# Kernel optimization log

Hardware: AMD Instinct MI355X
Metric: run time of the kernel (lower is better)

Reference implementation:

```python
import jax, jax.numpy as jnp
import numpy as np

T, H, I, E, K = 4096, 2048, 4096, 8, 2

def setup_inputs() -> dict:
    key = jax.random.key(0)
    k1, k2, k3, k4, k5 = jax.random.split(key, 5)
    return {
        "hidden_states": jax.random.normal(k1, (T, H), dtype=jnp.float32),
        "topk_weights": jax.random.uniform(k2, (T, K), dtype=jnp.float32, minval=0.01, maxval=1.0),
        "topk_ids": jax.random.randint(k3, (T, K), 0, E, dtype=jnp.int64),
        "gate_up_weights": jax.random.normal(k4, (E, 2 * I, H), dtype=jnp.float32) * 0.02,
        "down_weights": jax.random.normal(k5, (E, H, I), dtype=jnp.float32) * 0.02,
    }

def reference(hidden_states, topk_weights, topk_ids, gate_up_weights, down_weights):
    # renormalize=True: per-token top-k weights sum to 1
    tw = topk_weights / jnp.sum(topk_weights, axis=-1, keepdims=True)  # [T, K]
    n_experts = gate_up_weights.shape[0]
    # per-expert combine weight for each token: sum of tw where routed to expert e -> [E, T]
    expert_w = jax.vmap(
        lambda e: jnp.sum(jnp.where(topk_ids == e, tw, 0.0), axis=-1)
    )(jnp.arange(n_experts))

    def body(acc, ew):
        gu, dw, w = ew  # gu: [2I, H], dw: [H, I], w: [T]
        h = hidden_states @ gu.T            # [T, 2I]
        gate, up = jnp.split(h, 2, axis=-1)  # silu_and_mul epilogue
        act = jax.nn.silu(gate) * up        # [T, I]
        out_e = act @ dw.T                  # [T, H]
        return acc + w[:, None] * out_e, None

    init = jnp.zeros_like(hidden_states)
    out, _ = jax.lax.scan(body, init, (gate_up_weights, down_weights, expert_w))
    return out
```

## Files before the change

kernel.cpp:

```cpp
#include <hip/hip_runtime.h>


#define T_TOK 4096
#define H_DIM 2048
#define I_DIM 4096
#define E_NUM 8
#define K_TOP 2
#define NSLOT (T_TOK * K_TOP)

#define BM 128
#define BN 128
#define BK 64
#define LDK 72

typedef float f32x4 __attribute__((ext_vector_type(4)));
typedef __bf16 bf16x8 __attribute__((ext_vector_type(8)));
typedef unsigned int u32x4 __attribute__((ext_vector_type(4)));

static __device__ __forceinline__ unsigned short f2bf(float f) {
  unsigned u = __float_as_uint(f);
  u += 0x7FFFu + ((u >> 16) & 1u);
  return (unsigned short)(u >> 16);
}

static __device__ __forceinline__ unsigned long long pack4bf(float x0, float x1, float x2, float x3) {
  unsigned lo = (unsigned)f2bf(x0) | ((unsigned)f2bf(x1) << 16);
  unsigned hi = (unsigned)f2bf(x2) | ((unsigned)f2bf(x3) << 16);
  return (unsigned long long)lo | ((unsigned long long)hi << 32);
}

static __device__ __forceinline__ void gload16(void* lds, const void* g) {
  __builtin_amdgcn_global_load_lds(
      (const __attribute__((address_space(1))) unsigned int*)(g),
      (__attribute__((address_space(3))) unsigned int*)(lds), 16, 0, 0);
}

__global__ void routing_kernel(const float* __restrict__ tw,
                               const int* __restrict__ ids,
                               int* __restrict__ offsets,
                               int* __restrict__ stok,
                               float* __restrict__ sw,
                               int* __restrict__ slot_of) {
  __shared__ int cnt[E_NUM];
  __shared__ int cur[E_NUM];
  __shared__ int basesh[E_NUM + 1];
  int tid = threadIdx.x;
  if (tid < E_NUM) cnt[tid] = 0;
  __syncthreads();
  for (int idx = tid; idx < NSLOT; idx += 256) atomicAdd(&cnt[ids[idx]], 1);
  __syncthreads();
  if (tid == 0) {
    int acc = 0;
    for (int e = 0; e < E_NUM; ++e) { basesh[e] = acc; acc += cnt[e]; }
    basesh[E_NUM] = acc;
    for (int e = 0; e <= E_NUM; ++e) offsets[e] = basesh[e];
  }
  __syncthreads();
  if (tid < E_NUM) cur[tid] = basesh[tid];
  __syncthreads();
  for (int idx = tid; idx < NSLOT; idx += 256) {
    int t = idx >> 1;
    float w0 = tw[t * 2], w1 = tw[t * 2 + 1];
    float w = ((idx & 1) ? w1 : w0) / (w0 + w1);
    int e = ids[idx];
    int slot = atomicAdd(&cur[e], 1);
    stok[slot] = t;
    sw[slot] = w;
    slot_of[idx] = slot;
  }
}

__global__ __launch_bounds__(256) void cvt_bf16_kernel(const float* __restrict__ in,
                                                       unsigned short* __restrict__ out,
                                                       long long n8) {
  long long stride = (long long)gridDim.x * 256;
  for (long long i = (long long)blockIdx.x * 256 + threadIdx.x; i < n8; i += stride) {
    long long o = i * 8;
    f32x4 v0 = *(const f32x4*)(in + o);
    f32x4 v1 = *(const f32x4*)(in + o + 4);
    unsigned long long p0 = pack4bf(v0[0], v0[1], v0[2], v0[3]);
    unsigned long long p1 = pack4bf(v1[0], v1[1], v1[2], v1[3]);
    u32x4 st;
    st[0] = (unsigned)p0; st[1] = (unsigned)(p0 >> 32);
    st[2] = (unsigned)p1; st[3] = (unsigned)(p1 >> 32);
    *(u32x4*)(out + o) = st;
  }
}

__global__ __launch_bounds__(256, 2) void gemm1_bf16_kernel(
    const unsigned short* __restrict__ hb,
    const unsigned short* __restrict__ gub,
    const int* __restrict__ offsets, const int* __restrict__ stok,
    unsigned short* __restrict__ act) {
  int e = blockIdx.z;
  int base = offsets[e];
  int cnt = offsets[e + 1] - base;
  int m0 = blockIdx.y * BM;
  if (m0 >= cnt) return;
  int n0 = blockIdx.x * BN;
  int rem = cnt - m0;

  __shared__ __attribute__((aligned(16))) unsigned short As[BM * 64];
  __shared__ __attribute__((aligned(16))) unsigned short Bg[BN * 64];
  __shared__ __attribute__((aligned(16))) unsigned short Bu[BN * 64];
  __shared__ int toks[BM];

  int tid = threadIdx.x;
  if (tid < BM) toks[tid] = (tid < rem) ? stok[base + m0 + tid] : stok[base];
  __syncthreads();

  int lane = tid & 63;
  int wid = tid >> 6;
  int srow = lane >> 3;
  int scol = ((lane & 7) ^ srow) << 3;

  const unsigned short* wrow = gub + (size_t)e * (2 * (size_t)I_DIM) * H_DIM;
  const unsigned short* pa[4];
  const unsigned short* pg[4];
  const unsigned short* pu[4];
#pragma unroll
  for (int s = 0; s < 4; ++s) {
    int row = wid * 32 + s * 8 + srow;
    pa[s] = hb + (size_t)toks[row] * H_DIM + scol;
    pg[s] = wrow + (size_t)(n0 + row) * H_DIM + scol;
    pu[s] = wrow + (size_t)(I_DIM + n0 + row) * H_DIM + scol;
  }

  int lm = lane & 15;
  int q = lane >> 4;
  int wm = (wid >> 1) * 64;
  int wn = (wid & 1) * 64;
  int rc0 = ((q ^ (lm & 7)) << 3);
  int rc1 = (((4 + q) ^ (lm & 7)) << 3);

  f32x4 accg[4][4] = {};
  f32x4 accu[4][4] = {};

  for (int kb = 0; kb < H_DIM; kb += BK) {
#pragma unroll
    for (int s = 0; s < 4; ++s) {
      gload16(&As[(wid * 32 + s * 8) * 64], pa[s] + kb);
      gload16(&Bg[(wid * 32 + s * 8) * 64], pg[s] + kb);
      gload16(&Bu[(wid * 32 + s * 8) * 64], pu[s] + kb);
    }
    __syncthreads();
#pragma unroll
    for (int ks = 0; ks < 2; ++ks) {
      int ko = ks ? rc1 : rc0;
      bf16x8 a[4], bg[4], bu[4];
#pragma unroll
      for (int i = 0; i < 4; ++i)
        a[i] = *(const bf16x8*)&As[(wm + i * 16 + lm) * 64 + ko];
#pragma unroll
      for (int j = 0; j < 4; ++j) {
        bg[j] = *(const bf16x8*)&Bg[(wn + j * 16 + lm) * 64 + ko];
        bu[j] = *(const bf16x8*)&Bu[(wn + j * 16 + lm) * 64 + ko];
      }
#pragma unroll
      for (int i = 0; i < 4; ++i)
#pragma unroll
        for (int j = 0; j < 4; ++j) {
          accg[i][j] = __builtin_amdgcn_mfma_f32_16x16x32_bf16(a[i], bg[j], accg[i][j], 0, 0, 0);
          accu[i][j] = __builtin_amdgcn_mfma_f32_16x16x32_bf16(a[i], bu[j], accu[i][j], 0, 0, 0);
        }
    }
    __syncthreads();
  }

#pragma unroll
  for (int i = 0; i < 4; ++i) {
    int mb = wm + i * 16 + q * 4;
#pragma unroll
    for (int r = 0; r < 4; ++r) {
      int m = mb + r;
      if (m < rem) {
        size_t rowoff = (size_t)(base + m0 + m) * I_DIM + n0;
#pragma unroll
        for (int j = 0; j < 4; ++j) {
          int n = wn + j * 16 + lm;
          float g = accg[i][j][r];
          float u = accu[i][j][r];
          float aa = (g / (1.0f + __expf(-g))) * u;
          act[rowoff + n] = f2bf(aa);
        }
      }
    }
  }
}

__global__ __launch_bounds__(256, 2) void gemm2_bf16_kernel(
    const unsigned short* __restrict__ act, const unsigned short* __restrict__ dwb,
    const int* __restrict__ offsets, const float* __restrict__ sw,
    float* __restrict__ dout) {
  int e = blockIdx.z;
  int base = offsets[e];
  int cnt = offsets[e + 1] - base;
  int m0 = blockIdx.y * BM;
  if (m0 >= cnt) return;
  int n0 = blockIdx.x * BN;
  int rem = cnt - m0;

  __shared__ __attribute__((aligned(16))) unsigned short As[BM * 64];
  __shared__ __attribute__((aligned(16))) unsigned short Bs[BN * 64];
  __shared__ float wsl[BM];

  int tid = threadIdx.x;
  if (tid < BM) wsl[tid] = (tid < rem) ? sw[base + m0 + tid] : 0.f;

  int lane = tid & 63;
  int wid = tid >> 6;
  int srow = lane >> 3;
  int scol = ((lane & 7) ^ srow) << 3;

  const unsigned short* dp = dwb + (size_t)e * ((size_t)H_DIM * I_DIM);
  const unsigned short* pa[4];
  const unsigned short* pb[4];
#pragma unroll
  for (int s = 0; s < 4; ++s) {
    int row = wid * 32 + s * 8 + srow;
    pa[s] = act + (size_t)(base + m0 + row) * I_DIM + scol;
    pb[s] = dp + (size_t)(n0 + row) * I_DIM + scol;
  }

  int lm = lane & 15;
  int q = lane >> 4;
  int wm = (wid >> 1) * 64;
  int wn = (wid & 1) * 64;
  int rc0 = ((q ^ (lm & 7)) << 3);
  int rc1 = (((4 + q) ^ (lm & 7)) << 3);

  f32x4 acc[4][4] = {};

  for (int kb = 0; kb < I_DIM; kb += BK) {
#pragma unroll
    for (int s = 0; s < 4; ++s) {
      gload16(&As[(wid * 32 + s * 8) * 64], pa[s] + kb);
      gload16(&Bs[(wid * 32 + s * 8) * 64], pb[s] + kb);
    }
    __syncthreads();
#pragma unroll
    for (int ks = 0; ks < 2; ++ks) {
      int ko = ks ? rc1 : rc0;
      bf16x8 a[4], b[4];
#pragma unroll
      for (int i = 0; i < 4; ++i)
        a[i] = *(const bf16x8*)&As[(wm + i * 16 + lm) * 64 + ko];
#pragma unroll
      for (int j = 0; j < 4; ++j)
        b[j] = *(const bf16x8*)&Bs[(wn + j * 16 + lm) * 64 + ko];
#pragma unroll
      for (int i = 0; i < 4; ++i)
#pragma unroll
        for (int j = 0; j < 4; ++j)
          acc[i][j] = __builtin_amdgcn_mfma_f32_16x16x32_bf16(a[i], b[j], acc[i][j], 0, 0, 0);
    }
    __syncthreads();
  }

#pragma unroll
  for (int i = 0; i < 4; ++i) {
    int mb = wm + i * 16 + q * 4;
#pragma unroll
    for (int r = 0; r < 4; ++r) {
      int m = mb + r;
      if (m < rem) {
        float w = wsl[m];
        size_t rowoff = (size_t)(base + m0 + m) * H_DIM + n0;
#pragma unroll
        for (int j = 0; j < 4; ++j)
          dout[rowoff + wn + j * 16 + lm] = acc[i][j][r] * w;
      }
    }
  }
}

__global__ __launch_bounds__(256, 2) void gemm1_kernel(
    const float* __restrict__ hidden, const float* __restrict__ gu,
    const int* __restrict__ offsets, const int* __restrict__ stok,
    unsigned short* __restrict__ act) {
  int e = blockIdx.z;
  int base = offsets[e];
  int cnt = offsets[e + 1] - base;
  int m0 = blockIdx.y * BM;
  if (m0 >= cnt) return;
  int n0 = blockIdx.x * BN;
  int rem = cnt - m0;

  __shared__ unsigned short As[BM * LDK];
  __shared__ unsigned short Bg[BM * LDK];
  __shared__ unsigned short Bu[BM * LDK];
  __shared__ int toks[BM];

  int tid = threadIdx.x;
  if (tid < BM) toks[tid] = (tid < rem) ? stok[base + m0 + tid] : -1;
  __syncthreads();

  int lane = tid & 63;
  int wid = tid >> 6;
  int wm = (wid >> 1) * 64;
  int wn = (wid & 1) * 64;
  int lm = lane & 15;
  int q = lane >> 4;

  f32x4 accg[4][4] = {};
  f32x4 accu[4][4] = {};
  const float* gup = gu + (size_t)e * (2 * (size_t)I_DIM * H_DIM);

  for (int kb = 0; kb < H_DIM; kb += BK) {
#pragma unroll
    for (int s = 0; s < 8; ++s) {
      int task = tid + s * 256;
      int row = task >> 4;
      int cg = (task & 15) << 2;
      int tok = toks[row];
      float x0 = 0.f, x1 = 0.f, x2 = 0.f, x3 = 0.f;
      if (tok >= 0) {
        f32x4 v = *(const f32x4*)(hidden + (size_t)tok * H_DIM + kb + cg);
        x0 = v[0]; x1 = v[1]; x2 = v[2]; x3 = v[3];
      }
      *(unsigned long long*)&As[row * LDK + cg] = pack4bf(x0, x1, x2, x3);
    }
#pragma unroll
    for (int s = 0; s < 8; ++s) {
      int task = tid + s * 256;
      int row = task >> 4;
      int cg = (task & 15) << 2;
      f32x4 vg = *(const f32x4*)(gup + (size_t)(n0 + row) * H_DIM + kb + cg);
      f32x4 vu = *(const f32x4*)(gup + (size_t)(I_DIM + n0 + row) * H_DIM + kb + cg);
      *(unsigned long long*)&Bg[row * LDK + cg] = pack4bf(vg[0], vg[1], vg[2], vg[3]);
      *(unsigned long long*)&Bu[row * LDK + cg] = pack4bf(vu[0], vu[1], vu[2], vu[3]);
    }
    __syncthreads();
#pragma unroll
    for (int ks = 0; ks < 2; ++ks) {
      int ko = ks * 32 + q * 8;
      bf16x8 a[4], bg[4], bu[4];
#pragma unroll
      for (int i = 0; i < 4; ++i)
        a[i] = *(const bf16x8*)&As[(wm + i * 16 + lm) * LDK + ko];
#pragma unroll
      for (int j = 0; j < 4; ++j) {
        bg[j] = *(const bf16x8*)&Bg[(wn + j * 16 + lm) * LDK + ko];
        bu[j] = *(const bf16x8*)&Bu[(wn + j * 16 + lm) * LDK + ko];
      }
#pragma unroll
      for (int i = 0; i < 4; ++i)
#pragma unroll
        for (int j = 0; j < 4; ++j) {
          accg[i][j] = __builtin_amdgcn_mfma_f32_16x16x32_bf16(a[i], bg[j], accg[i][j], 0, 0, 0);
          accu[i][j] = __builtin_amdgcn_mfma_f32_16x16x32_bf16(a[i], bu[j], accu[i][j], 0, 0, 0);
        }
    }
    __syncthreads();
  }

#pragma unroll
  for (int i = 0; i < 4; ++i) {
    int mb = wm + i * 16 + q * 4;
#pragma unroll
    for (int r = 0; r < 4; ++r) {
      int m = mb + r;
      if (m < rem) {
        size_t rowoff = (size_t)(base + m0 + m) * I_DIM + n0;
#pragma unroll
        for (int j = 0; j < 4; ++j) {
          int n = wn + j * 16 + lm;
          float g = accg[i][j][r];
          float u = accu[i][j][r];
          float aa = (g / (1.0f + __expf(-g))) * u;
          act[rowoff + n] = f2bf(aa);
        }
      }
    }
  }
}

__global__ __launch_bounds__(256, 2) void gemm2_kernel(
    const unsigned short* __restrict__ act, const float* __restrict__ dwn,
    const int* __restrict__ offsets, const float* __restrict__ sw,
    float* __restrict__ dout) {
  int e = blockIdx.z;
  int base = offsets[e];
  int cnt = offsets[e + 1] - base;
  int m0 = blockIdx.y * BM;
  if (m0 >= cnt) return;
  int n0 = blockIdx.x * BN;
  int rem = cnt - m0;

  __shared__ unsigned short As[BM * LDK];
  __shared__ unsigned short Bs[BM * LDK];
  __shared__ float wsl[BM];

  int tid = threadIdx.x;
  if (tid < BM) wsl[tid] = (tid < rem) ? sw[base + m0 + tid] : 0.f;

  int lane = tid & 63;
  int wid = tid >> 6;
  int wm = (wid >> 1) * 64;
  int wn = (wid & 1) * 64;
  int lm = lane & 15;
  int q = lane >> 4;

  f32x4 acc[4][4] = {};
  const float* dp = dwn + (size_t)e * ((size_t)H_DIM * I_DIM);
  const unsigned short* ap = act + (size_t)(base + m0) * I_DIM;

  for (int kb = 0; kb < I_DIM; kb += BK) {
#pragma unroll
    for (int s = 0; s < 4; ++s) {
      int task = tid + s * 256;
      int row = task >> 3;
      int cg = (task & 7) << 3;
      u32x4 v = *(const u32x4*)(ap + (size_t)row * I_DIM + kb + cg);
      *(u32x4*)&As[row * LDK + cg] = v;
    }
#pragma unroll
    for (int s = 0; s < 8; ++s) {
      int task = tid + s * 256;
      int row = task >> 4;
      int cg = (task & 15) << 2;
      f32x4 v = *(const f32x4*)(dp + (size_t)(n0 + row) * I_DIM + kb + cg);
      *(unsigned long long*)&Bs[row * LDK + cg] = pack4bf(v[0], v[1], v[2], v[3]);
    }
    __syncthreads();
#pragma unroll
    for (int ks = 0; ks < 2; ++ks) {
      int ko = ks * 32 + q * 8;
      bf16x8 a[4], b[4];
#pragma unroll
      for (int i = 0; i < 4; ++i)
        a[i] = *(const bf16x8*)&As[(wm + i * 16 + lm) * LDK + ko];
#pragma unroll
      for (int j = 0; j < 4; ++j)
        b[j] = *(const bf16x8*)&Bs[(wn + j * 16 + lm) * LDK + ko];
#pragma unroll
      for (int i = 0; i < 4; ++i)
#pragma unroll
        for (int j = 0; j < 4; ++j)
          acc[i][j] = __builtin_amdgcn_mfma_f32_16x16x32_bf16(a[i], b[j], acc[i][j], 0, 0, 0);
    }
    __syncthreads();
  }

#pragma unroll
  for (int i = 0; i < 4; ++i) {
    int mb = wm + i * 16 + q * 4;
#pragma unroll
    for (int r = 0; r < 4; ++r) {
      int m = mb + r;
      if (m < rem) {
        float w = wsl[m];
        size_t rowoff = (size_t)(base + m0 + m) * H_DIM + n0;
#pragma unroll
        for (int j = 0; j < 4; ++j)
          dout[rowoff + wn + j * 16 + lm] = acc[i][j][r] * w;
      }
    }
  }
}

__global__ void combine_kernel(const f32x4* __restrict__ dout4,
                               const int* __restrict__ slot_of,
                               f32x4* __restrict__ out4) {
  int idx = blockIdx.x * 256 + threadIdx.x;
  int t = idx >> 9;
  int c = idx & 511;
  int s0 = slot_of[t * 2];
  int s1 = slot_of[t * 2 + 1];
  f32x4 r = dout4[(size_t)s0 * 512 + c] + dout4[(size_t)s1 * 512 + c];
  out4[idx] = r;
}

extern "C" void kernel_launch(void* const* d_in, const int* in_sizes, int n_in,
                              void* d_out, int out_size, void* d_ws, size_t ws_size,
                              hipStream_t stream) {
  const float* hidden = (const float*)d_in[0];
  const float* tw     = (const float*)d_in[1];
  const int*   ids    = (const int*)d_in[2];
  const float* gu     = (const float*)d_in[3];
  const float* dwn    = (const float*)d_in[4];
  float* out = (float*)d_out;
  char* ws = (char*)d_ws;

  int*   offsets = (int*)ws;
  int*   stok    = (int*)(ws + 256);
  float* swp     = (float*)(ws + 256 + 32768);
  int*   slot_of = (int*)(ws + 256 + 65536);
  const size_t base_off = 1 << 17;
  const size_t act_sz   = (size_t)(NSLOT + BM) * I_DIM * 2;

  routing_kernel<<<1, 256, 0, stream>>>(tw, ids, offsets, stok, swp, slot_of);

  const size_t hb_sz  = (size_t)T_TOK * H_DIM * 2;
  const size_t gu_sz  = (size_t)E_NUM * 2 * (size_t)I_DIM * H_DIM * 2;
  const size_t dwn_sz = (size_t)E_NUM * (size_t)H_DIM * I_DIM * 2;
  const size_t w_off  = base_off + hb_sz;
  const size_t need   = w_off + gu_sz + act_sz;

  if (ws_size >= need) {
    unsigned short* hb   = (unsigned short*)(ws + base_off);
    unsigned short* gub  = (unsigned short*)(ws + w_off);
    unsigned short* dwb  = (unsigned short*)(ws + w_off);
    float*          dout = (float*)(ws + w_off + dwn_sz);
    unsigned short* act  = (unsigned short*)(ws + w_off + gu_sz);

    cvt_bf16_kernel<<<4096, 256, 0, stream>>>(hidden, hb, (long long)T_TOK * H_DIM / 8);
    cvt_bf16_kernel<<<8192, 256, 0, stream>>>(gu, gub, (long long)E_NUM * 2 * I_DIM * H_DIM / 8);
    gemm1_bf16_kernel<<<dim3(I_DIM / BN, NSLOT / BM, E_NUM), 256, 0, stream>>>(hb, gub, offsets, stok, act);
    cvt_bf16_kernel<<<8192, 256, 0, stream>>>(dwn, dwb, (long long)E_NUM * H_DIM * I_DIM / 8);
    gemm2_bf16_kernel<<<dim3(H_DIM / BN, NSLOT / BM, E_NUM), 256, 0, stream>>>(act, dwb, offsets, swp, dout);
    combine_kernel<<<(T_TOK * H_DIM / 4) / 256, 256, 0, stream>>>((const f32x4*)dout, slot_of, (f32x4*)out);
  } else {
    unsigned short* act  = (unsigned short*)(ws + base_off);
    float*          dout = (float*)(ws + base_off + act_sz);
    gemm1_kernel<<<dim3(I_DIM / BN, NSLOT / BM, E_NUM), 256, 0, stream>>>(hidden, gu, offsets, stok, act);
    gemm2_kernel<<<dim3(H_DIM / BN, NSLOT / BM, E_NUM), 256, 0, stream>>>(act, dwn, offsets, swp, dout);
    combine_kernel<<<(T_TOK * H_DIM / 4) / 256, 256, 0, stream>>>((const f32x4*)dout, slot_of, (f32x4*)out);
  }
}
```

Before: 1.480 ms.

## Double-buffer LDS tiles with BK=32 prefetch in bf16 expert GEMMs

Converts the bf16 gate-up and down GEMM kernels from a single-buffered BK=64 load/sync/compute loop to a double-buffered BK=32 loop. The next K-slice is issued to the alternate LDS buffer before computing on the current one, so there is one barrier per iteration instead of two. Each kernel keeps about the same LDS footprint. The swizzle is reworked for 32-wide rows, and gemm2's launch bounds rise to 3 blocks per CU to allow more occupancy. The trade-off is twice as many loop iterations and barriers per K range, and possible register pressure from the higher occupancy target. The fp32 fallback kernels only get the renamed stride constant and a hardcoded 64-step.

Measured after the change: 1.607 ms. 8.6% more time.

```diff
diff --git a/kernel.cpp b/kernel.cpp
--- a/kernel.cpp
+++ b/kernel.cpp
@@ -10,8 +10,8 @@
 
 #define BM 128
 #define BN 128
-#define BK 64
-#define LDK 72
+#define BK 32
+#define LDKO 72
 
 typedef float f32x4 __attribute__((ext_vector_type(4)));
 typedef __bf16 bf16x8 __attribute__((ext_vector_type(8)));
@@ -100,9 +100,9 @@
   int n0 = blockIdx.x * BN;
   int rem = cnt - m0;
 
-  __shared__ __attribute__((aligned(16))) unsigned short As[BM * 64];
-  __shared__ __attribute__((aligned(16))) unsigned short Bg[BN * 64];
-  __shared__ __attribute__((aligned(16))) unsigned short Bu[BN * 64];
+  __shared__ __attribute__((aligned(16))) unsigned short As[2][BM * BK];
+  __shared__ __attribute__((aligned(16))) unsigned short Bg[2][BN * BK];
+  __shared__ __attribute__((aligned(16))) unsigned short Bu[2][BN * BK];
   __shared__ int toks[BM];
 
   int tid = threadIdx.x;
@@ -111,60 +111,70 @@
 
   int lane = tid & 63;
   int wid = tid >> 6;
-  int srow = lane >> 3;
-  int scol = ((lane & 7) ^ srow) << 3;
+  int sr = lane >> 2;
+  int scz = ((lane & 3) ^ (sr & 3)) << 3;
 
   const unsigned short* wrow = gub + (size_t)e * (2 * (size_t)I_DIM) * H_DIM;
-  const unsigned short* pa[4];
-  const unsigned short* pg[4];
-  const unsigned short* pu[4];
-#pragma unroll
-  for (int s = 0; s < 4; ++s) {
-    int row = wid * 32 + s * 8 + srow;
-    pa[s] = hb + (size_t)toks[row] * H_DIM + scol;
-    pg[s] = wrow + (size_t)(n0 + row) * H_DIM + scol;
-    pu[s] = wrow + (size_t)(I_DIM + n0 + row) * H_DIM + scol;
+  const unsigned short* pa[2];
+  const unsigned short* pg[2];
+  const unsigned short* pu[2];
+  int lb[2];
+#pragma unroll
+  for (int s = 0; s < 2; ++s) {
+    int grp = (wid * 2 + s) * 16;
+    int row = grp + sr;
+    pa[s] = hb + (size_t)toks[row] * H_DIM + scz;
+    pg[s] = wrow + (size_t)(n0 + row) * H_DIM + scz;
+    pu[s] = wrow + (size_t)(I_DIM + n0 + row) * H_DIM + scz;
+    lb[s] = grp * BK;
   }
 
   int lm = lane & 15;
   int q = lane >> 4;
   int wm = (wid >> 1) * 64;
   int wn = (wid & 1) * 64;
-  int rc0 = ((q ^ (lm & 7)) << 3);
-  int rc1 = (((4 + q) ^ (lm & 7)) << 3);
+  int rcs = ((q ^ (lm & 3)) << 3);
 
   f32x4 accg[4][4] = {};
   f32x4 accu[4][4] = {};
 
+#pragma unroll
+  for (int s = 0; s < 2; ++s) {
+    gload16(&As[0][lb[s]], pa[s]);
+    gload16(&Bg[0][lb[s]], pg[s]);
+    gload16(&Bu[0][lb[s]], pu[s]);
+  }
+  __syncthreads();
+
+  int cur = 0;
   for (int kb = 0; kb < H_DIM; kb += BK) {
-#pragma unroll
-    for (int s = 0; s < 4; ++s) {
-      gload16(&As[(wid * 32 + s * 8) * 64], pa[s] + kb);
-      gload16(&Bg[(wid * 32 + s * 8) * 64], pg[s] + kb);
-      gload16(&Bu[(wid * 32 + s * 8) * 64], pu[s] + kb);
-    }
+    if (kb + BK < H_DIM) {
+      int nk = kb + BK;
+#pragma unroll
+      for (int s = 0; s < 2; ++s) {
+        gload16(&As[cur ^ 1][lb[s]], pa[s] + nk);
+        gload16(&Bg[cur ^ 1][lb[s]], pg[s] + nk);
+        gload16(&Bu[cur ^ 1][lb[s]], pu[s] + nk);
+      }
+    }
+    bf16x8 a[4], bg[4], bu[4];
+#pragma unroll
+    for (int i = 0; i < 4; ++i)
+      a[i] = *(const bf16x8*)&As[cur][(wm + i * 16 + lm) * BK + rcs];
+#pragma unroll
+    for (int j = 0; j < 4; ++j) {
+      bg[j] = *(const bf16x8*)&Bg[cur][(wn + j * 16 + lm) * BK + rcs];
+      bu[j] = *(const bf16x8*)&Bu[cur][(wn + j * 16 + lm) * BK + rcs];
+    }
+#pragma unroll
+    for (int i = 0; i < 4; ++i)
+#pragma unroll
+      for (int j = 0; j < 4; ++j) {
+        accg[i][j] = __builtin_amdgcn_mfma_f32_16x16x32_bf16(a[i], bg[j], accg[i][j], 0, 0, 0);
+        accu[i][j] = __builtin_amdgcn_mfma_f32_16x16x32_bf16(a[i], bu[j], accu[i][j], 0, 0, 0);
+      }
     __syncthreads();
-#pragma unroll
-    for (int ks = 0; ks < 2; ++ks) {
-      int ko = ks ? rc1 : rc0;
-      bf16x8 a[4], bg[4], bu[4];
-#pragma unroll
-      for (int i = 0; i < 4; ++i)
-        a[i] = *(const bf16x8*)&As[(wm + i * 16 + lm) * 64 + ko];
-#pragma unroll
-      for (int j = 0; j < 4; ++j) {
-        bg[j] = *(const bf16x8*)&Bg[(wn + j * 16 + lm) * 64 + ko];
-        bu[j] = *(const bf16x8*)&Bu[(wn + j * 16 + lm) * 64 + ko];
-      }
-#pragma unroll
-      for (int i = 0; i < 4; ++i)
-#pragma unroll
-        for (int j = 0; j < 4; ++j) {
-          accg[i][j] = __builtin_amdgcn_mfma_f32_16x16x32_bf16(a[i], bg[j], accg[i][j], 0, 0, 0);
-          accu[i][j] = __builtin_amdgcn_mfma_f32_16x16x32_bf16(a[i], bu[j], accu[i][j], 0, 0, 0);
-        }
-    }
-    __syncthreads();
+    cur ^= 1;
   }
 
 #pragma unroll
@@ -188,7 +198,7 @@
   }
 }
 
-__global__ __launch_bounds__(256, 2) void gemm2_bf16_kernel(
+__global__ __launch_bounds__(256, 3) void gemm2_bf16_kernel(
     const unsigned short* __restrict__ act, const unsigned short* __restrict__ dwb,
     const int* __restrict__ offsets, const float* __restrict__ sw,
     float* __restrict__ dout) {
@@ -200,8 +210,8 @@
   int n0 = blockIdx.x * BN;
   int rem = cnt - m0;
 
-  __shared__ __attribute__((aligned(16))) unsigned short As[BM * 64];
-  __shared__ __attribute__((aligned(16))) unsigned short Bs[BN * 64];
+  __shared__ __attribute__((aligned(16))) unsigned short As[2][BM * BK];
+  __shared__ __attribute__((aligned(16))) unsigned short Bs[2][BN * BK];
   __shared__ float wsl[BM];
 
   int tid = threadIdx.x;
@@ -209,52 +219,61 @@
 
   int lane = tid & 63;
   int wid = tid >> 6;
-  int srow = lane >> 3;
-  int scol = ((lane & 7) ^ srow) << 3;
+  int sr = lane >> 2;
+  int scz = ((lane & 3) ^ (sr & 3)) << 3;
 
   const unsigned short* dp = dwb + (size_t)e * ((size_t)H_DIM * I_DIM);
-  const unsigned short* pa[4];
-  const unsigned short* pb[4];
-#pragma unroll
-  for (int s = 0; s < 4; ++s) {
-    int row = wid * 32 + s * 8 + srow;
-    pa[s] = act + (size_t)(base + m0 + row) * I_DIM + scol;
-    pb[s] = dp + (size_t)(n0 + row) * I_DIM + scol;
+  const unsigned short* pa[2];
+  const unsigned short* pb[2];
+  int lb[2];
+#pragma unroll
+  for (int s = 0; s < 2; ++s) {
+    int grp = (wid * 2 + s) * 16;
+    int row = grp + sr;
+    pa[s] = act + (size_t)(base + m0 + row) * I_DIM + scz;
+    pb[s] = dp + (size_t)(n0 + row) * I_DIM + scz;
+    lb[s] = grp * BK;
   }
 
   int lm = lane & 15;
   int q = lane >> 4;
   int wm = (wid >> 1) * 64;
   int wn = (wid & 1) * 64;
-  int rc0 = ((q ^ (lm & 7)) << 3);
-  int rc1 = (((4 + q) ^ (lm & 7)) << 3);
+  int rcs = ((q ^ (lm & 3)) << 3);
 
   f32x4 acc[4][4] = {};
 
+#pragma unroll
+  for (int s = 0; s < 2; ++s) {
+    gload16(&As[0][lb[s]], pa[s]);
+    gload16(&Bs[0][lb[s]], pb[s]);
+  }
+  __syncthreads();
+
+  int cur = 0;
   for (int kb = 0; kb < I_DIM; kb += BK) {
-#pragma unroll
-    for (int s = 0; s < 4; ++s) {
-      gload16(&As[(wid * 32 + s * 8) * 64], pa[s] + kb);
-      gload16(&Bs[(wid * 32 + s * 8) * 64], pb[s] + kb);
-    }
+    if (kb + BK < I_DIM) {
+      int nk = kb + BK;
+#pragma unroll
+      for (int s = 0; s < 2; ++s) {
+        gload16(&As[cur ^ 1][lb[s]], pa[s] + nk);
+        gload16(&Bs[cur ^ 1][lb[s]], pb[s] + nk);
+      }
+    }
+    bf16x8 a[4], b[4];
+#pragma unroll
+    for (int i = 0; i < 4; ++i)
+      a[i] = *(const bf16x8*)&As[cur][(wm + i * 16 + lm) * BK + rcs];
+#pragma unroll
+    for (int j = 0; j < 4; ++j)
+      b[j] = *(const bf16x8*)&Bs[cur][(wn + j * 16 + lm) * BK + rcs];
+#pragma unroll
+    for (int i = 0; i < 4; ++i)
+#pragma unroll
+      for (int j = 0; j < 4; ++j)
+        acc[i][j] = __builtin_amdgcn_mfma_f32_16x16x32_bf16(a[i], b[j], acc[i][j], 0, 0, 0);
     __syncthreads();
-#pragma unroll
-    for (int ks = 0; ks < 2; ++ks) {
-      int ko = ks ? rc1 : rc0;
-      bf16x8 a[4], b[4];
-#pragma unroll
-      for (int i = 0; i < 4; ++i)
-        a[i] = *(const bf16x8*)&As[(wm + i * 16 + lm) * 64 + ko];
-#pragma unroll
-      for (int j = 0; j < 4; ++j)
-        b[j] = *(const bf16x8*)&Bs[(wn + j * 16 + lm) * 64 + ko];
-#pragma unroll
-      for (int i = 0; i < 4; ++i)
-#pragma unroll
-        for (int j = 0; j < 4; ++j)
-          acc[i][j] = __builtin_amdgcn_mfma_f32_16x16x32_bf16(a[i], b[j], acc[i][j], 0, 0, 0);
-    }
-    __syncthreads();
+    cur ^= 1;
   }
 
 #pragma unroll
@@ -286,9 +305,9 @@
   int n0 = blockIdx.x * BN;
   int rem = cnt - m0;
 
-  __shared__ unsigned short As[BM * LDK];
-  __shared__ unsigned short Bg[BM * LDK];
-  __shared__ unsigned short Bu[BM * LDK];
+  __shared__ unsigned short As[BM * LDKO];
+  __shared__ unsigned short Bg[BM * LDKO];
+  __shared__ unsigned short Bu[BM * LDKO];
   __shared__ int toks[BM];
 
   int tid = threadIdx.x;
@@ -306,7 +325,7 @@
   f32x4 accu[4][4] = {};
   const float* gup = gu + (size_t)e * (2 * (size_t)I_DIM * H_DIM);
 
-  for (int kb = 0; kb < H_DIM; kb += BK) {
+  for (int kb = 0; kb < H_DIM; kb += 64) {
 #pragma unroll
     for (int s = 0; s < 8; ++s) {
       int task = tid + s * 256;
@@ -318,7 +337,7 @@
         f32x4 v = *(const f32x4*)(hidden + (size_t)tok * H_DIM + kb + cg);
         x0 = v[0]; x1 = v[1]; x2 = v[2]; x3 = v[3];
       }
-      *(unsigned long long*)&As[row * LDK + cg] = pack4bf(x0, x1, x2, x3);
+      *(unsigned long long*)&As[row * LDKO + cg] = pack4bf(x0, x1, x2, x3);
     }
 #pragma unroll
     for (int s = 0; s < 8; ++s) {
@@ -327,8 +346,8 @@
       int cg = (task & 15) << 2;
       f32x4 vg = *(const f32x4*)(gup + (size_t)(n0 + row) * H_DIM + kb + cg);
       f32x4 vu = *(const f32x4*)(gup + (size_t)(I_DIM + n0 + row) * H_DIM + kb + cg);
-      *(unsigned long long*)&Bg[row * LDK + cg] = pack4bf(vg[0], vg[1], vg[2], vg[3]);
-      *(unsigned long long*)&Bu[row * LDK + cg] = pack4bf(vu[0], vu[1], vu[2], vu[3]);
+      *(unsigned long long*)&Bg[row * LDKO + cg] = pack4bf(vg[0], vg[1], vg[2], vg[3]);
+      *(unsigned long long*)&Bu[row * LDKO + cg] = pack4bf(vu[0], vu[1], vu[2], vu[3]);
     }
     __syncthreads();
 #pragma unroll
@@ -337,11 +356,11 @@
       bf16x8 a[4], bg[4], bu[4];
 #pragma unroll
       for (int i = 0; i < 4; ++i)
-        a[i] = *(const bf16x8*)&As[(wm + i * 16 + lm) * LDK + ko];
+        a[i] = *(const bf16x8*)&As[(wm + i * 16 + lm) * LDKO + ko];
 #pragma unroll
       for (int j = 0; j < 4; ++j) {
-        bg[j] = *(const bf16x8*)&Bg[(wn + j * 16 + lm) * LDK + ko];
-        bu[j] = *(const bf16x8*)&Bu[(wn + j * 16 + lm) * LDK + ko];
+        bg[j] = *(const bf16x8*)&Bg[(wn + j * 16 + lm) * LDKO + ko];
+        bu[j] = *(const bf16x8*)&Bu[(wn + j * 16 + lm) * LDKO + ko];
       }
 #pragma unroll
       for (int i = 0; i < 4; ++i)
@@ -387,8 +406,8 @@
   int n0 = blockIdx.x * BN;
   int rem = cnt - m0;
 
-  __shared__ unsigned short As[BM * LDK];
-  __shared__ unsigned short Bs[BM * LDK];
+  __shared__ unsigned short As[BM * LDKO];
+  __shared__ unsigned short Bs[BM * LDKO];
   __shared__ float wsl[BM];
 
   int tid = threadIdx.x;
@@ -405,14 +424,14 @@
   const float* dp = dwn + (size_t)e * ((size_t)H_DIM * I_DIM);
   const unsigned short* ap = act + (size_t)(base + m0) * I_DIM;
 
-  for (int kb = 0; kb < I_DIM; kb += BK) {
+  for (int kb = 0; kb < I_DIM; kb += 64) {
 #pragma unroll
     for (int s = 0; s < 4; ++s) {
       int task = tid + s * 256;
       int row = task >> 3;
       int cg = (task & 7) << 3;
       u32x4 v = *(const u32x4*)(ap + (size_t)row * I_DIM + kb + cg);
-      *(u32x4*)&As[row * LDK + cg] = v;
+      *(u32x4*)&As[row * LDKO + cg] = v;
     }
 #pragma unroll
     for (int s = 0; s < 8; ++s) {
@@ -420,7 +439,7 @@
       int row = task >> 4;
       int cg = (task & 15) << 2;
       f32x4 v = *(const f32x4*)(dp + (size_t)(n0 + row) * I_DIM + kb + cg);
-      *(unsigned long long*)&Bs[row * LDK + cg] = pack4bf(v[0], v[1], v[2], v[3]);
+      *(unsigned long long*)&Bs[row * LDKO + cg] = pack4bf(v[0], v[1], v[2], v[3]);
     }
     __syncthreads();
 #pragma unroll
@@ -429,10 +448,10 @@
       bf16x8 a[4], b[4];
 #pragma unroll
       for (int i = 0; i < 4; ++i)
-        a[i] = *(const bf16x8*)&As[(wm + i * 16 + lm) * LDK + ko];
+        a[i] = *(const bf16x8*)&As[(wm + i * 16 + lm) * LDKO + ko];
 #pragma unroll
       for (int j = 0; j < 4; ++j)
-        b[j] = *(const bf16x8*)&Bs[(wn + j * 16 + lm) * LDK + ko];
+        b[j] = *(const bf16x8*)&Bs[(wn + j * 16 + lm) * LDKO + ko];
 #pragma unroll
       for (int i = 0; i < 4; ++i)
 #pragma unroll
```
